# Optimization experiments

Hardware: AMD Instinct MI355X
Metric: run time of the kernel (lower is better)

## Reference

```python
import jax, jax.numpy as jnp
import numpy as np

B, S, HID = 2, 1024, 4096
NQ, NG, D = 32, 4, 128
NKV = NQ // NG  # 8 kv heads
OFF = 1024


def setup_inputs() -> dict:
    key = jax.random.key(0)
    ks = jax.random.split(key, 13)
    w = 0.02
    return {
        "x": jax.random.normal(ks[0], (B, S, HID), jnp.float32),
        "offset": OFF,
        "precomp_freqs_cos": jax.random.uniform(ks[1], (S, D // 2), jnp.float32, -1.0, 1.0),
        "precomp_freqs_sin": jax.random.uniform(ks[2], (S, D // 2), jnp.float32, -1.0, 1.0),
        "k_cache": jax.random.normal(ks[3], (B, OFF, NQ, D), jnp.float32),
        "v_cache": jax.random.normal(ks[4], (B, OFF, NQ, D), jnp.float32),
        "q_w": jax.random.normal(ks[5], (NQ * D, HID), jnp.float32) * w,
        "q_b": jax.random.normal(ks[6], (NQ * D,), jnp.float32) * w,
        "k_w": jax.random.normal(ks[7], (NKV * D, HID), jnp.float32) * w,
        "k_b": jax.random.normal(ks[8], (NKV * D,), jnp.float32) * w,
        "v_w": jax.random.normal(ks[9], (NKV * D, HID), jnp.float32) * w,
        "v_b": jax.random.normal(ks[10], (NKV * D,), jnp.float32) * w,
        "o_w": jax.random.normal(ks[11], (HID, NQ * D), jnp.float32) * w,
    }


def _rope(x, cos, sin):
    # x: [b, s, h, d]; cos/sin: [s, d//2] applied to interleaved pairs
    b, s, h, d = x.shape
    xp = x.reshape(b, s, h, d // 2, 2)
    xr, xi = xp[..., 0], xp[..., 1]
    c = cos[None, :, None, :]
    sn = sin[None, :, None, :]
    out = jnp.stack([xr * c - xi * sn, xr * sn + xi * c], axis=-1)
    return out.reshape(b, s, h, d)


def reference(x, offset, precomp_freqs_cos, precomp_freqs_sin, k_cache, v_cache,
              q_w, q_b, k_w, k_b, v_w, v_b, o_w):
    b, s, _ = x.shape
    q = (x @ q_w.T + q_b).reshape(b, s, NQ, D)
    k = (x @ k_w.T + k_b).reshape(b, s, NKV, D)
    v = (x @ v_w.T + v_b).reshape(b, s, NKV, D)
    # GQA expansion: '(hr)' -> each kv head repeated NG times contiguously
    k = jnp.repeat(k, NG, axis=2)  # [b, s, NQ, D]
    v = jnp.repeat(v, NG, axis=2)
    q = _rope(q, precomp_freqs_cos, precomp_freqs_sin)
    k = _rope(k, precomp_freqs_cos, precomp_freqs_sin)
    k = jnp.concatenate([k_cache, k], axis=1)  # [b, offset+s, NQ, D]
    v = jnp.concatenate([v_cache, v], axis=1)
    qk = jnp.einsum('bsnd,btnd->bnst', q, k) / np.float32(np.sqrt(D))
    neg_inf = jnp.asarray(-jnp.inf, qk.dtype)
    causal = jnp.triu(jnp.full((s, s), neg_inf, qk.dtype), k=1)
    mask = jnp.concatenate([jnp.zeros((s, offset), qk.dtype), causal], axis=1)
    qk = qk + mask[None, None, :, :]
    p = jax.nn.softmax(qk, axis=-1)
    out = jnp.einsum('bnst,btnd->bsnd', p, v).reshape(b, s, NQ * D)
    out = out @ o_w.T
    return (out, k, v)
```

## Files before the change

### kernel.cpp

```cpp
#include <hip/hip_runtime.h>
#include <hip/hip_bf16.h>
#include <cstdio>
#include <cstdint>

typedef __bf16 bf16_t;
typedef __bf16 bf16x8 __attribute__((ext_vector_type(8)));
typedef float f32x4 __attribute__((ext_vector_type(4)));

static constexpr int Bc = 2, Sc = 1024, HIDc = 4096;
static constexpr int NQc = 32, NKVc = 8, Dc = 128, OFFc = 1024, Tc = 2048;
static constexpr int Mrows = Bc * Sc;
static constexpr int NQKV = (NQc + 2 * NKVc) * Dc;

__device__ inline void load_lds16(const void* g, void* l) {
    __builtin_amdgcn_global_load_lds(
        (const __attribute__((address_space(1))) unsigned*)g,
        (__attribute__((address_space(3))) unsigned*)l, 16, 0, 0);
}

__global__ void k_cvt5(const float* __restrict__ s0, const float* __restrict__ s1,
                       const float* __restrict__ s2, const float* __restrict__ s3,
                       const float* __restrict__ s4,
                       bf16_t* __restrict__ d0, bf16_t* __restrict__ d1,
                       bf16_t* __restrict__ d2, bf16_t* __restrict__ d3,
                       bf16_t* __restrict__ d4,
                       long c0, long c1, long c2, long c3, long c4) {
    long i = blockIdx.x * (long)blockDim.x + threadIdx.x;
    long stride = (long)gridDim.x * blockDim.x;
    for (; i < c4; i += stride) {
        const float* src; bf16_t* dst; long j;
        if (i < c0)      { src = s0; dst = d0; j = i; }
        else if (i < c1) { src = s1; dst = d1; j = i - c0; }
        else if (i < c2) { src = s2; dst = d2; j = i - c1; }
        else if (i < c3) { src = s3; dst = d3; j = i - c2; }
        else             { src = s4; dst = d4; j = i - c3; }
        float4 v = *(const float4*)&src[j * 4];
        bf16_t t[4] = {(bf16_t)v.x, (bf16_t)v.y, (bf16_t)v.z, (bf16_t)v.w};
        *(uint2*)&dst[j * 4] = *(uint2*)t;
    }
}

template <int BM, bool BIAS, bool OUT_BF16>
__global__ __launch_bounds__(256) void k_gemm(const bf16_t* __restrict__ A,
                                              const bf16_t* __restrict__ Bm,
                                              const float* __restrict__ bias,
                                              void* __restrict__ Cout,
                                              int M, int N, int K) {
    constexpr int MI = BM / 32;
    __shared__ __align__(16) bf16_t As[BM][64];
    __shared__ __align__(16) bf16_t Bs[128][64];
    const int tid = threadIdx.x, wid = tid >> 6, lane = tid & 63;
    const int g = lane >> 4, ln = lane & 15;
    const int wm = wid >> 1, wn = wid & 1;
    const int gx = gridDim.x;
    int bidl = blockIdx.y * gx + blockIdx.x;
    int cpx = (gx * gridDim.y) >> 3;
    int swz = (bidl & 7) * cpx + (bidl >> 3);
    const int m0 = (swz / gx) * BM, n0 = (swz % gx) * 128;
    f32x4 acc[MI][4] = {};

    for (int k0 = 0; k0 < K; k0 += 64) {
        __syncthreads();
#pragma unroll
        for (int c = 0; c < BM / 32; ++c) {
            int row = wid * (BM / 4) + c * 8 + (lane >> 3);
            int col = ((lane & 7) ^ (row & 7)) * 8;
            load_lds16(A + (size_t)(m0 + row) * K + k0 + col, &As[wid * (BM / 4) + c * 8][0]);
        }
#pragma unroll
        for (int c = 0; c < 4; ++c) {
            int row = wid * 32 + c * 8 + (lane >> 3);
            int col = ((lane & 7) ^ (row & 7)) * 8;
            load_lds16(Bm + (size_t)(n0 + row) * K + k0 + col, &Bs[wid * 32 + c * 8][0]);
        }
        __syncthreads();
#pragma unroll
        for (int kk = 0; kk < 2; ++kk) {
            bf16x8 af[MI], bfr[4];
#pragma unroll
            for (int i = 0; i < MI; ++i) {
                int row = wm * (BM / 2) + i * 16 + ln;
                af[i] = *(const bf16x8*)&As[row][(((kk * 4 + g) ^ (row & 7)) * 8)];
            }
#pragma unroll
            for (int j = 0; j < 4; ++j) {
                int row = wn * 64 + j * 16 + ln;
                bfr[j] = *(const bf16x8*)&Bs[row][(((kk * 4 + g) ^ (row & 7)) * 8)];
            }
#pragma unroll
            for (int i = 0; i < MI; ++i)
#pragma unroll
                for (int j = 0; j < 4; ++j)
                    acc[i][j] = __builtin_amdgcn_mfma_f32_16x16x32_bf16(af[i], bfr[j], acc[i][j], 0, 0, 0);
        }
    }

#pragma unroll
    for (int i = 0; i < MI; ++i) {
#pragma unroll
        for (int j = 0; j < 4; ++j) {
            int col = n0 + wn * 64 + j * 16 + ln;
            float bv = BIAS ? bias[col] : 0.f;
#pragma unroll
            for (int r = 0; r < 4; ++r) {
                int row = m0 + wm * (BM / 2) + i * 16 + g * 4 + r;
                float v = acc[i][j][r] + bv;
                if (OUT_BF16)
                    ((bf16_t*)Cout)[(size_t)row * N + col] = (bf16_t)v;
                else
                    ((float*)Cout)[(size_t)row * N + col] = v;
            }
        }
    }
}

__global__ void k_rope_q(bf16_t* __restrict__ qkv, const float* __restrict__ cosT,
                         const float* __restrict__ sinT) {
    int row = blockIdx.x;
    int s = row & 1023;
    bf16_t* src = qkv + (size_t)row * NQKV;
    for (int p = threadIdx.x; p < 2048; p += 256) {
        int j = p & 63;
        float c = cosT[s * 64 + j], sn = sinT[s * 64 + j];
        float xr = (float)src[2 * p], xi = (float)src[2 * p + 1];
        src[2 * p]     = (bf16_t)(xr * c - xi * sn);
        src[2 * p + 1] = (bf16_t)(xr * sn + xi * c);
    }
}


__global__ __launch_bounds__(256) void k_ropekv(const bf16_t* __restrict__ qkv,
                                                const float* __restrict__ cosT,
                                                const float* __restrict__ sinT,
                                                float* __restrict__ out_k,
                                                float* __restrict__ out_v,
                                                bf16_t* __restrict__ kfr,
                                                bf16_t* __restrict__ vfr) {
    __shared__ __align__(16) bf16_t Vl[64][136];
    const int sb = blockIdx.x, hk = blockIdx.y, b = blockIdx.z;
    const int tid = threadIdx.x;
    const int tt = tid >> 2, dq = (tid & 3) * 32;
    const int s = sb * 64 + tt;
    const int t = OFFc + s;
    const bf16_t* krow = qkv + (size_t)(b * Sc + s) * NQKV + NQc * Dc + hk * Dc + dq;
    const bf16_t* vrow = qkv + (size_t)(b * Sc + s) * NQKV + (NQc + NKVc) * Dc + hk * Dc + dq;

    float cs[16], sn[16];
    int j0 = dq >> 1;
#pragma unroll
    for (int q4 = 0; q4 < 4; ++q4) {
        float4 cv = *(const float4*)&cosT[s * 64 + j0 + q4 * 4];
        float4 sv = *(const float4*)&sinT[s * 64 + j0 + q4 * 4];
        cs[q4 * 4] = cv.x; cs[q4 * 4 + 1] = cv.y; cs[q4 * 4 + 2] = cv.z; cs[q4 * 4 + 3] = cv.w;
        sn[q4 * 4] = sv.x; sn[q4 * 4 + 1] = sv.y; sn[q4 * 4 + 2] = sv.z; sn[q4 * 4 + 3] = sv.w;
    }

    bf16_t kb[32], vb[32];
#pragma unroll
    for (int c = 0; c < 4; ++c) {
        *(uint4*)&kb[c * 8] = *(const uint4*)&krow[c * 8];
        *(uint4*)&vb[c * 8] = *(const uint4*)&vrow[c * 8];
    }
    float ko[32], vo[32];
    bf16_t kbf[32];
#pragma unroll
    for (int jj = 0; jj < 16; ++jj) {
        float xr = (float)kb[2 * jj], xi = (float)kb[2 * jj + 1];
        ko[2 * jj]     = xr * cs[jj] - xi * sn[jj];
        ko[2 * jj + 1] = xr * sn[jj] + xi * cs[jj];
        kbf[2 * jj]     = (bf16_t)ko[2 * jj];
        kbf[2 * jj + 1] = (bf16_t)ko[2 * jj + 1];
        vo[2 * jj] = (float)vb[2 * jj];
        vo[2 * jj + 1] = (float)vb[2 * jj + 1];
    }

    const int t16 = t >> 4, lnr = t & 15, dc = dq >> 5;
#pragma unroll
    for (int gg = 0; gg < 4; ++gg) {
        int hq = hk * 4 + gg;
        size_t o = ((size_t)(b * Tc + t) * NQc + hq) * Dc + dq;
#pragma unroll
        for (int c = 0; c < 8; ++c) {
            *(float4*)&out_k[o + c * 4] = *(float4*)&ko[c * 4];
            *(float4*)&out_v[o + c * 4] = *(float4*)&vo[c * 4];
        }
        size_t fb = ((size_t)b * NQc + hq) * ((size_t)Tc * Dc);
#pragma unroll
        for (int g = 0; g < 4; ++g)
            *(uint4*)&kfr[fb + (size_t)(((t16 * 4 + dc) * 4 + g) * 128 + lnr * 8)] = *(uint4*)&kbf[g * 8];
    }
#pragma unroll
    for (int c = 0; c < 4; ++c) *(uint4*)&Vl[tt][dq + c * 8] = *(uint4*)&vb[c * 8];
    __syncthreads();
    const int tile = 16 + sb;
#pragma unroll
    for (int i = 0; i < 4; ++i) {
        int u = i * 256 + tid;
        int d = u >> 3, cc = u & 7;
        bf16_t tmp[8];
#pragma unroll
        for (int j = 0; j < 8; ++j) tmp[j] = Vl[cc * 8 + j][d];
        size_t off = (size_t)((((tile * 8 + (d >> 4)) * 2 + (cc >> 2)) * 4 + (cc & 3)) * 128 + (d & 15) * 8);
#pragma unroll
        for (int gg = 0; gg < 4; ++gg) {
            int hq = hk * 4 + gg;
            size_t fb = ((size_t)b * NQc + hq) * ((size_t)Tc * Dc);
            *(uint4*)&vfr[fb + off] = *(uint4*)tmp;
        }
    }
}

__global__ __launch_bounds__(256) void k_cache(const float* __restrict__ kc,
                                               const float* __restrict__ vc,
                                               float* __restrict__ out_k,
                                               float* __restrict__ out_v,
                                               bf16_t* __restrict__ kfr,
                                               bf16_t* __restrict__ vfr) {
    __shared__ __align__(16) bf16_t Vl[64][136];
    const int tb = blockIdx.x, h = blockIdx.y, b = blockIdx.z;
    const int tid = threadIdx.x;
    const int tt = tid >> 2, dq = (tid & 3) * 32;
    const int t = tb * 64 + tt;
    size_t src = ((size_t)(b * OFFc + t) * NQc + h) * Dc + dq;
    size_t dst = ((size_t)(b * Tc + t) * NQc + h) * Dc + dq;
    const size_t fb = ((size_t)b * NQc + h) * ((size_t)Tc * Dc);

    bf16_t kb[32], vb[32];
#pragma unroll
    for (int c = 0; c < 8; ++c) {
        float4 kv = *(const float4*)&kc[src + c * 4];
        *(float4*)&out_k[dst + c * 4] = kv;
        kb[c * 4] = (bf16_t)kv.x; kb[c * 4 + 1] = (bf16_t)kv.y;
        kb[c * 4 + 2] = (bf16_t)kv.z; kb[c * 4 + 3] = (bf16_t)kv.w;
        float4 vv = *(const float4*)&vc[src + c * 4];
        *(float4*)&out_v[dst + c * 4] = vv;
        vb[c * 4] = (bf16_t)vv.x; vb[c * 4 + 1] = (bf16_t)vv.y;
        vb[c * 4 + 2] = (bf16_t)vv.z; vb[c * 4 + 3] = (bf16_t)vv.w;
    }
    const int t16 = t >> 4, lnr = t & 15, dc = dq >> 5;
#pragma unroll
    for (int g = 0; g < 4; ++g)
        *(uint4*)&kfr[fb + (size_t)(((t16 * 4 + dc) * 4 + g) * 128 + lnr * 8)] = *(uint4*)&kb[g * 8];

#pragma unroll
    for (int c = 0; c < 4; ++c) *(uint4*)&Vl[tt][dq + c * 8] = *(uint4*)&vb[c * 8];
    __syncthreads();
#pragma unroll
    for (int i = 0; i < 4; ++i) {
        int u = i * 256 + tid;
        int d = u >> 3, cc = u & 7;
        bf16_t tmp[8];
#pragma unroll
        for (int j = 0; j < 8; ++j) tmp[j] = Vl[cc * 8 + j][d];
        size_t off = (size_t)((((tb * 8 + (d >> 4)) * 2 + (cc >> 2)) * 4 + (cc & 3)) * 128 + (d & 15) * 8);
        *(uint4*)&vfr[fb + off] = *(uint4*)tmp;
    }
}

__global__ __launch_bounds__(512) void k_attn(const bf16_t* __restrict__ qkv,
                                              const bf16_t* __restrict__ kfr,
                                              const bf16_t* __restrict__ vfr,
                                              bf16_t* __restrict__ attn) {
    __shared__ __align__(16) bf16_t Kl[2][8192];
    __shared__ __align__(16) bf16_t Vl2[2][8192];
    __shared__ __align__(16) bf16_t Pl[8][32 * 72];
    const int tid = threadIdx.x, w = tid >> 6, l = tid & 63;
    const int g = l >> 4, ln = l & 15;
    const int bid = blockIdx.x;
    const int xcd = bid & 7, within = bid >> 3;
    const int qblk = 3 - (within & 3);
    const int u = within >> 2;
    const int b = u >> 2;
    const int h = (u & 3) * 8 + xcd;
    const int q0b = qblk * 256;
    const int qw0 = q0b + w * 32;
    const float SCALE = 0.08838834764831845f;
    const float L2E = 1.4426950408889634f;
    const size_t hb = ((size_t)b * NQc + h) * ((size_t)Tc * Dc);
    const bf16_t* kb = kfr + hb;
    const bf16_t* vb = vfr + hb;
    bf16_t* Pw = &Pl[w][0];

    bf16x8 qf[2][4];
#pragma unroll
    for (int mf = 0; mf < 2; ++mf) {
        size_t qrow = (size_t)(b * Sc + qw0 + mf * 16 + ln) * NQKV + h * Dc;
#pragma unroll
        for (int dc = 0; dc < 4; ++dc) qf[mf][dc] = *(const bf16x8*)&qkv[qrow + dc * 32 + g * 8];
    }
    f32x4 o[2][8] = {};
    float mrun[2] = {-1e30f, -1e30f};
    float lrun[2] = {0.f, 0.f};

    const int ntiles = (OFFc + q0b + 256) >> 6;

    auto stage = [&](int bf, int t) {
        const bf16_t* ksrc = kb + (size_t)t * 8192 + (size_t)(w * 2) * 512;
        const bf16_t* vsrc = vb + (size_t)t * 8192 + (size_t)(w * 2) * 512;
        load_lds16(ksrc + (size_t)l * 8,       &Kl[bf][(w * 2) * 512]);
        load_lds16(ksrc + 512 + (size_t)l * 8, &Kl[bf][(w * 2 + 1) * 512]);
        load_lds16(vsrc + (size_t)l * 8,       &Vl2[bf][(w * 2) * 512]);
        load_lds16(vsrc + 512 + (size_t)l * 8, &Vl2[bf][(w * 2 + 1) * 512]);
    };

    stage(0, 0);
    __syncthreads();
    int cur = 0;

    for (int t = 0; t < ntiles; ++t) {
        if (t + 1 < ntiles) stage(cur ^ 1, t + 1);
        f32x4 sa[2][4] = {};
#pragma unroll
        for (int nf = 0; nf < 4; ++nf) {
            bf16x8 kf[4];
#pragma unroll
            for (int dc = 0; dc < 4; ++dc)
                kf[dc] = *(const bf16x8*)&Kl[cur][((nf * 4 + dc) * 4 + g) * 128 + ln * 8];
#pragma unroll
            for (int dc = 0; dc < 4; ++dc) {
                sa[0][nf] = __builtin_amdgcn_mfma_f32_16x16x32_bf16(kf[dc], qf[0][dc], sa[0][nf], 0, 0, 0);
                sa[1][nf] = __builtin_amdgcn_mfma_f32_16x16x32_bf16(kf[dc], qf[1][dc], sa[1][nf], 0, 0, 0);
            }
        }
        bool maybe = (t * 64 + 63 > OFFc + qw0);
#pragma unroll
        for (int mf = 0; mf < 2; ++mf)
#pragma unroll
            for (int nf = 0; nf < 4; ++nf)
#pragma unroll
                for (int r = 0; r < 4; ++r) {
                    float s = sa[mf][nf][r] * SCALE;
                    if (maybe) {
                        int tg = t * 64 + nf * 16 + g * 4 + r;
                        int qg = qw0 + mf * 16 + ln;
                        if (tg > OFFc + qg) s = -1e30f;
                    }
                    sa[mf][nf][r] = s;
                }
        float tm[2];
        int grew = 0;
#pragma unroll
        for (int mf = 0; mf < 2; ++mf) {
            float m2 = sa[mf][0][0];
#pragma unroll
            for (int nf = 0; nf < 4; ++nf)
#pragma unroll
                for (int r = 0; r < 4; ++r) m2 = fmaxf(m2, sa[mf][nf][r]);
            m2 = fmaxf(m2, __shfl_xor(m2, 16));
            m2 = fmaxf(m2, __shfl_xor(m2, 32));
            tm[mf] = m2;
            grew |= (m2 > mrun[mf]) ? 1 : 0;
        }
        if (__any(grew)) {
#pragma unroll
            for (int mf = 0; mf < 2; ++mf) {
                float mn = fmaxf(mrun[mf], tm[mf]);
                float al = exp2f((mrun[mf] - mn) * L2E);
                mrun[mf] = mn;
                lrun[mf] *= al;
                float alr[4];
#pragma unroll
                for (int r = 0; r < 4; ++r)
                    alr[r] = __shfl(al, (l & 48) | (g * 4 + r));
#pragma unroll
                for (int df = 0; df < 8; ++df) {
                    f32x4 t4 = o[mf][df];
                    t4[0] *= alr[0]; t4[1] *= alr[1]; t4[2] *= alr[2]; t4[3] *= alr[3];
                    o[mf][df] = t4;
                }
            }
        }
#pragma unroll
        for (int mf = 0; mf < 2; ++mf) {
            const int qrow = mf * 16 + ln;
            float ps = 0.f;
#pragma unroll
            for (int nf = 0; nf < 4; ++nf) {
                bf16_t pv[4];
#pragma unroll
                for (int r = 0; r < 4; ++r) {
                    float p = exp2f((sa[mf][nf][r] - mrun[mf]) * L2E);
                    ps += p;
                    pv[r] = (bf16_t)p;
                }
                *(uint2*)&Pw[qrow * 72 + nf * 16 + g * 4] = *(uint2*)pv;
            }
            ps += __shfl_xor(ps, 16);
            ps += __shfl_xor(ps, 32);
            lrun[mf] += ps;
        }
#pragma unroll
        for (int kc = 0; kc < 2; ++kc) {
            bf16x8 vf[8];
#pragma unroll
            for (int df = 0; df < 8; ++df)
                vf[df] = *(const bf16x8*)&Vl2[cur][((df * 2 + kc) * 4 + g) * 128 + ln * 8];
#pragma unroll
            for (int mf = 0; mf < 2; ++mf) {
                bf16x8 pa = *(const bf16x8*)&Pw[(mf * 16 + ln) * 72 + kc * 32 + g * 8];
#pragma unroll
                for (int df = 0; df < 8; ++df)
                    o[mf][df] = __builtin_amdgcn_mfma_f32_16x16x32_bf16(pa, vf[df], o[mf][df], 0, 0, 0);
            }
        }
        __syncthreads();
        cur ^= 1;
    }

#pragma unroll
    for (int mf = 0; mf < 2; ++mf) {
        float linv[4];
#pragma unroll
        for (int r = 0; r < 4; ++r)
            linv[r] = 1.f / __shfl(lrun[mf], (l & 48) | (g * 4 + r));
#pragma unroll
        for (int df = 0; df < 8; ++df)
#pragma unroll
            for (int r = 0; r < 4; ++r) {
                float v = o[mf][df][r] * linv[r];
                size_t orow = (size_t)(b * Sc + qw0 + mf * 16 + g * 4 + r) * (NQc * Dc) + h * Dc + df * 16 + ln;
                attn[orow] = (bf16_t)v;
            }
    }
}

extern "C" void kernel_launch(void* const* d_in, const int* in_sizes, int n_in,
                              void* d_out, int out_size, void* d_ws, size_t ws_size,
                              hipStream_t stream) {
    const float* x      = (const float*)d_in[0];
    const float* cosT   = (const float*)d_in[2];
    const float* sinT   = (const float*)d_in[3];
    const float* kcache = (const float*)d_in[4];
    const float* vcache = (const float*)d_in[5];
    const float* q_w    = (const float*)d_in[6];
    const float* q_b    = (const float*)d_in[7];
    const float* k_w    = (const float*)d_in[8];
    const float* k_b    = (const float*)d_in[9];
    const float* v_w    = (const float*)d_in[10];
    const float* v_b    = (const float*)d_in[11];
    const float* o_w    = (const float*)d_in[12];

    char* ws = (char*)d_ws;
    size_t off = 0;
    auto alloc = [&](size_t bytes) {
        void* p = ws + off;
        off += (bytes + 255) & ~(size_t)255;
        return p;
    };
    bf16_t* xb   = (bf16_t*)alloc((size_t)Mrows * HIDc * 2);
    bf16_t* wqkv = (bf16_t*)alloc((size_t)Bc * Tc * NQc * Dc * 4);
    bf16_t* owb  = (bf16_t*)alloc((size_t)HIDc * HIDc * 2);
    bf16_t* qkv  = (bf16_t*)alloc((size_t)Mrows * NQKV * 2);
    float*  bias = (float*)alloc((size_t)NQKV * 4);
    if (off > ws_size) {
        fprintf(stderr, "WS too small: need %zu have %zu\n", off, ws_size);
        return;
    }
    bf16_t* attn  = xb;
    bf16_t* kfr = wqkv;
    bf16_t* vfr = wqkv + (size_t)Bc * NQc * Tc * Dc;

    float* out_o = (float*)d_out;
    float* out_k = out_o + (size_t)Mrows * HIDc;
    float* out_v = out_k + (size_t)Bc * Tc * NQc * Dc;

    const long n0 = (long)Mrows * HIDc / 4;
    const long n1 = (long)NQc * Dc * HIDc / 4;
    const long n2 = (long)NKVc * Dc * HIDc / 4;
    const long n4 = (long)HIDc * HIDc / 4;
    k_cvt5<<<4096, 256, 0, stream>>>(
        x, q_w, k_w, v_w, o_w,
        xb, wqkv, wqkv + (size_t)NQc * Dc * HIDc, wqkv + (size_t)(NQc + NKVc) * Dc * HIDc, owb,
        n0, n0 + n1, n0 + n1 + n2, n0 + n1 + 2 * n2, n0 + n1 + 2 * n2 + n4);
    (void)hipMemcpyAsync(bias, q_b, (size_t)NQc * Dc * 4, hipMemcpyDeviceToDevice, stream);
    (void)hipMemcpyAsync(bias + NQc * Dc, k_b, (size_t)NKVc * Dc * 4, hipMemcpyDeviceToDevice, stream);
    (void)hipMemcpyAsync(bias + (NQc + NKVc) * Dc, v_b, (size_t)NKVc * Dc * 4, hipMemcpyDeviceToDevice, stream);

    k_gemm<128, true, true><<<dim3(NQKV / 128, Mrows / 128), 256, 0, stream>>>(
        xb, wqkv, bias, qkv, Mrows, NQKV, HIDc);
    k_rope_q<<<Mrows, 256, 0, stream>>>(qkv, cosT, sinT);
    k_ropekv<<<dim3(16, 8, 2), 256, 0, stream>>>(qkv, cosT, sinT, out_k, out_v, kfr, vfr);
    k_cache<<<dim3(16, 32, 2), 256, 0, stream>>>(kcache, vcache, out_k, out_v, kfr, vfr);
    k_attn<<<256, 512, 0, stream>>>(qkv, kfr, vfr, attn);
    k_gemm<64, false, false><<<dim3(HIDc / 128, Mrows / 64), 256, 0, stream>>>(
        attn, owb, nullptr, d_out, Mrows, HIDc, HIDc);
}
```

Measured before the change: 470.5 us.

## Shrink attention blocks to 128 queries with register-staged single-buffer K/V loads

```diff
diff --git a/kernel.cpp b/kernel.cpp
--- a/kernel.cpp
+++ b/kernel.cpp
@@ -257,22 +257,22 @@
     }
 }
 
-__global__ __launch_bounds__(512) void k_attn(const bf16_t* __restrict__ qkv,
+__global__ __launch_bounds__(256) void k_attn(const bf16_t* __restrict__ qkv,
                                               const bf16_t* __restrict__ kfr,
                                               const bf16_t* __restrict__ vfr,
                                               bf16_t* __restrict__ attn) {
-    __shared__ __align__(16) bf16_t Kl[2][8192];
-    __shared__ __align__(16) bf16_t Vl2[2][8192];
-    __shared__ __align__(16) bf16_t Pl[8][32 * 72];
+    __shared__ __align__(16) bf16_t Kl[8192];
+    __shared__ __align__(16) bf16_t Vl2[8192];
+    __shared__ __align__(16) bf16_t Pl[4][32 * 72];
     const int tid = threadIdx.x, w = tid >> 6, l = tid & 63;
     const int g = l >> 4, ln = l & 15;
     const int bid = blockIdx.x;
     const int xcd = bid & 7, within = bid >> 3;
-    const int qblk = 3 - (within & 3);
-    const int u = within >> 2;
+    const int qblk = 7 - (within & 7);
+    const int u = within >> 3;
     const int b = u >> 2;
     const int h = (u & 3) * 8 + xcd;
-    const int q0b = qblk * 256;
+    const int q0b = qblk * 128;
     const int qw0 = q0b + w * 32;
     const float SCALE = 0.08838834764831845f;
     const float L2E = 1.4426950408889634f;
@@ -292,119 +292,134 @@
     float mrun[2] = {-1e30f, -1e30f};
     float lrun[2] = {0.f, 0.f};
 
-    const int ntiles = (OFFc + q0b + 256) >> 6;
-
-    auto stage = [&](int bf, int t) {
-        const bf16_t* ksrc = kb + (size_t)t * 8192 + (size_t)(w * 2) * 512;
-        const bf16_t* vsrc = vb + (size_t)t * 8192 + (size_t)(w * 2) * 512;
-        load_lds16(ksrc + (size_t)l * 8,       &Kl[bf][(w * 2) * 512]);
-        load_lds16(ksrc + 512 + (size_t)l * 8, &Kl[bf][(w * 2 + 1) * 512]);
-        load_lds16(vsrc + (size_t)l * 8,       &Vl2[bf][(w * 2) * 512]);
-        load_lds16(vsrc + 512 + (size_t)l * 8, &Vl2[bf][(w * 2 + 1) * 512]);
+    const int ntiles = (OFFc + q0b + 128) >> 6;
+    const int lastw = (OFFc + qw0 + 31) >> 6;
+
+    bf16x8 kp[4], vp[4];
+    auto prefetch = [&](int t) {
+        const bf16_t* ks = kb + (size_t)t * 8192 + w * 2048;
+        const bf16_t* vs = vb + (size_t)t * 8192 + w * 2048;
+#pragma unroll
+        for (int c = 0; c < 4; ++c) {
+            kp[c] = *(const bf16x8*)&ks[c * 512 + l * 8];
+            vp[c] = *(const bf16x8*)&vs[c * 512 + l * 8];
+        }
     };
-
-    stage(0, 0);
+    auto commit = [&]() {
+#pragma unroll
+        for (int c = 0; c < 4; ++c) {
+            *(bf16x8*)&Kl[w * 2048 + c * 512 + l * 8] = kp[c];
+            *(bf16x8*)&Vl2[w * 2048 + c * 512 + l * 8] = vp[c];
+        }
+    };
+
+    prefetch(0);
+    commit();
     __syncthreads();
-    int cur = 0;
 
     for (int t = 0; t < ntiles; ++t) {
-        if (t + 1 < ntiles) stage(cur ^ 1, t + 1);
-        f32x4 sa[2][4] = {};
-#pragma unroll
-        for (int nf = 0; nf < 4; ++nf) {
-            bf16x8 kf[4];
-#pragma unroll
-            for (int dc = 0; dc < 4; ++dc)
-                kf[dc] = *(const bf16x8*)&Kl[cur][((nf * 4 + dc) * 4 + g) * 128 + ln * 8];
-#pragma unroll
-            for (int dc = 0; dc < 4; ++dc) {
-                sa[0][nf] = __builtin_amdgcn_mfma_f32_16x16x32_bf16(kf[dc], qf[0][dc], sa[0][nf], 0, 0, 0);
-                sa[1][nf] = __builtin_amdgcn_mfma_f32_16x16x32_bf16(kf[dc], qf[1][dc], sa[1][nf], 0, 0, 0);
-            }
-        }
-        bool maybe = (t * 64 + 63 > OFFc + qw0);
-#pragma unroll
-        for (int mf = 0; mf < 2; ++mf)
-#pragma unroll
-            for (int nf = 0; nf < 4; ++nf)
-#pragma unroll
-                for (int r = 0; r < 4; ++r) {
-                    float s = sa[mf][nf][r] * SCALE;
-                    if (maybe) {
-                        int tg = t * 64 + nf * 16 + g * 4 + r;
-                        int qg = qw0 + mf * 16 + ln;
-                        if (tg > OFFc + qg) s = -1e30f;
+        if (t + 1 < ntiles) prefetch(t + 1);
+        if (t <= lastw) {
+            f32x4 sa[2][4] = {};
+#pragma unroll
+            for (int nf = 0; nf < 4; ++nf) {
+                bf16x8 kf[4];
+#pragma unroll
+                for (int dc = 0; dc < 4; ++dc)
+                    kf[dc] = *(const bf16x8*)&Kl[((nf * 4 + dc) * 4 + g) * 128 + ln * 8];
+#pragma unroll
+                for (int dc = 0; dc < 4; ++dc) {
+                    sa[0][nf] = __builtin_amdgcn_mfma_f32_16x16x32_bf16(kf[dc], qf[0][dc], sa[0][nf], 0, 0, 0);
+                    sa[1][nf] = __builtin_amdgcn_mfma_f32_16x16x32_bf16(kf[dc], qf[1][dc], sa[1][nf], 0, 0, 0);
+                }
+            }
+            bool maybe = (t * 64 + 63 > OFFc + qw0);
+#pragma unroll
+            for (int mf = 0; mf < 2; ++mf)
+#pragma unroll
+                for (int nf = 0; nf < 4; ++nf)
+#pragma unroll
+                    for (int r = 0; r < 4; ++r) {
+                        float s = sa[mf][nf][r] * SCALE;
+                        if (maybe) {
+                            int tg = t * 64 + nf * 16 + g * 4 + r;
+                            int qg = qw0 + mf * 16 + ln;
+                            if (tg > OFFc + qg) s = -1e30f;
+                        }
+                        sa[mf][nf][r] = s;
                     }
-                    sa[mf][nf][r] = s;
+            float tm[2];
+            int grew = 0;
+#pragma unroll
+            for (int mf = 0; mf < 2; ++mf) {
+                float m2 = sa[mf][0][0];
+#pragma unroll
+                for (int nf = 0; nf < 4; ++nf)
+#pragma unroll
+                    for (int r = 0; r < 4; ++r) m2 = fmaxf(m2, sa[mf][nf][r]);
+                m2 = fmaxf(m2, __shfl_xor(m2, 16));
+                m2 = fmaxf(m2, __shfl_xor(m2, 32));
+                tm[mf] = m2;
+                grew |= (m2 > mrun[mf]) ? 1 : 0;
+            }
+            if (__any(grew)) {
+#pragma unroll
+                for (int mf = 0; mf < 2; ++mf) {
+                    float mn = fmaxf(mrun[mf], tm[mf]);
+                    float al = exp2f((mrun[mf] - mn) * L2E);
+                    mrun[mf] = mn;
+                    lrun[mf] *= al;
+                    float alr[4];
+#pragma unroll
+                    for (int r = 0; r < 4; ++r)
+                        alr[r] = __shfl(al, (l & 48) | (g * 4 + r));
+#pragma unroll
+                    for (int df = 0; df < 8; ++df) {
+                        f32x4 t4 = o[mf][df];
+                        t4[0] *= alr[0]; t4[1] *= alr[1]; t4[2] *= alr[2]; t4[3] *= alr[3];
+                        o[mf][df] = t4;
+                    }
                 }
-        float tm[2];
-        int grew = 0;
-#pragma unroll
-        for (int mf = 0; mf < 2; ++mf) {
-            float m2 = sa[mf][0][0];
-#pragma unroll
-            for (int nf = 0; nf < 4; ++nf)
-#pragma unroll
-                for (int r = 0; r < 4; ++r) m2 = fmaxf(m2, sa[mf][nf][r]);
-            m2 = fmaxf(m2, __shfl_xor(m2, 16));
-            m2 = fmaxf(m2, __shfl_xor(m2, 32));
-            tm[mf] = m2;
-            grew |= (m2 > mrun[mf]) ? 1 : 0;
-        }
-        if (__any(grew)) {
+            }
 #pragma unroll
             for (int mf = 0; mf < 2; ++mf) {
-                float mn = fmaxf(mrun[mf], tm[mf]);
-                float al = exp2f((mrun[mf] - mn) * L2E);
-                mrun[mf] = mn;
-                lrun[mf] *= al;
-                float alr[4];
-#pragma unroll
-                for (int r = 0; r < 4; ++r)
-                    alr[r] = __shfl(al, (l & 48) | (g * 4 + r));
-#pragma unroll
-                for (int df = 0; df < 8; ++df) {
-                    f32x4 t4 = o[mf][df];
-                    t4[0] *= alr[0]; t4[1] *= alr[1]; t4[2] *= alr[2]; t4[3] *= alr[3];
-                    o[mf][df] = t4;
+                const int qrow = mf * 16 + ln;
+                float ps = 0.f;
+#pragma unroll
+                for (int nf = 0; nf < 4; ++nf) {
+                    bf16_t pv[4];
+#pragma unroll
+                    for (int r = 0; r < 4; ++r) {
+                        float p = exp2f((sa[mf][nf][r] - mrun[mf]) * L2E);
+                        ps += p;
+                        pv[r] = (bf16_t)p;
+                    }
+                    *(uint2*)&Pw[qrow * 72 + nf * 16 + g * 4] = *(uint2*)pv;
                 }
-            }
-        }
-#pragma unroll
-        for (int mf = 0; mf < 2; ++mf) {
-            const int qrow = mf * 16 + ln;
-            float ps = 0.f;
-#pragma unroll
-            for (int nf = 0; nf < 4; ++nf) {
-                bf16_t pv[4];
-#pragma unroll
-                for (int r = 0; r < 4; ++r) {
-                    float p = exp2f((sa[mf][nf][r] - mrun[mf]) * L2E);
-                    ps += p;
-                    pv[r] = (bf16_t)p;
+                ps += __shfl_xor(ps, 16);
+                ps += __shfl_xor(ps, 32);
+                lrun[mf] += ps;
+            }
+#pragma unroll
+            for (int kc = 0; kc < 2; ++kc) {
+                bf16x8 vf[8];
+#pragma unroll
+                for (int df = 0; df < 8; ++df)
+                    vf[df] = *(const bf16x8*)&Vl2[((df * 2 + kc) * 4 + g) * 128 + ln * 8];
+#pragma unroll
+                for (int mf = 0; mf < 2; ++mf) {
+                    bf16x8 pa = *(const bf16x8*)&Pw[(mf * 16 + ln) * 72 + kc * 32 + g * 8];
+#pragma unroll
+                    for (int df = 0; df < 8; ++df)
+                        o[mf][df] = __builtin_amdgcn_mfma_f32_16x16x32_bf16(pa, vf[df], o[mf][df], 0, 0, 0);
                 }
-                *(uint2*)&Pw[qrow * 72 + nf * 16 + g * 4] = *(uint2*)pv;
-            }
-            ps += __shfl_xor(ps, 16);
-            ps += __shfl_xor(ps, 32);
-            lrun[mf] += ps;
-        }
-#pragma unroll
-        for (int kc = 0; kc < 2; ++kc) {
-            bf16x8 vf[8];
-#pragma unroll
-            for (int df = 0; df < 8; ++df)
-                vf[df] = *(const bf16x8*)&Vl2[cur][((df * 2 + kc) * 4 + g) * 128 + ln * 8];
-#pragma unroll
-            for (int mf = 0; mf < 2; ++mf) {
-                bf16x8 pa = *(const bf16x8*)&Pw[(mf * 16 + ln) * 72 + kc * 32 + g * 8];
-#pragma unroll
-                for (int df = 0; df < 8; ++df)
-                    o[mf][df] = __builtin_amdgcn_mfma_f32_16x16x32_bf16(pa, vf[df], o[mf][df], 0, 0, 0);
             }
         }
         __syncthreads();
-        cur ^= 1;
+        if (t + 1 < ntiles) {
+            commit();
+        }
+        __syncthreads();
     }
 
 #pragma unroll
@@ -481,7 +496,7 @@
     k_rope_q<<<Mrows, 256, 0, stream>>>(qkv, cosT, sinT);
     k_ropekv<<<dim3(16, 8, 2), 256, 0, stream>>>(qkv, cosT, sinT, out_k, out_v, kfr, vfr);
     k_cache<<<dim3(16, 32, 2), 256, 0, stream>>>(kcache, vcache, out_k, out_v, kfr, vfr);
-    k_attn<<<256, 512, 0, stream>>>(qkv, kfr, vfr, attn);
+    k_attn<<<512, 256, 0, stream>>>(qkv, kfr, vfr, attn);
     k_gemm<64, false, false><<<dim3(HIDc / 128, Mrows / 64), 256, 0, stream>>>(
         attn, owb, nullptr, d_out, Mrows, HIDc, HIDc);
 }
```

New measurement: 545.6 us. 16.0% more time.
